# Optimization experiments

Hardware: AMD Instinct MI355X
Metric: run time of the kernel (lower is better)

## Reference

```python
import jax, jax.numpy as jnp
import numpy as np

B, N, C, H = 2, 2048, 768, 12  # batch, seq, dim_self, num_heads
HD = C // H                    # head_dim = 64


def setup_inputs() -> dict:
    key = jax.random.key(0)
    ks = jax.random.split(key, 6)
    s = 0.02
    return {
        "x": jax.random.normal(ks[0], (B, N, C), jnp.float32),
        "mask": jax.random.bernoulli(ks[1], 0.9, (B, N)),  # True = attend (code applies ~mask)
        "Wq": jax.random.normal(ks[2], (C, C), jnp.float32) * s,
        "bq": jnp.zeros((C,), jnp.float32),
        "Wkv": jax.random.normal(ks[3], (C, 2 * C), jnp.float32) * s,
        "bkv": jnp.zeros((2 * C,), jnp.float32),
        "Wp": jax.random.normal(ks[4], (C, C), jnp.float32) * s,
        "bp": jnp.zeros((C,), jnp.float32),
    }


def reference(x, mask, Wq, bq, Wkv, bkv, Wp, bp):
    b, n, c = x.shape
    scale = HD ** -0.5
    # projections (self-attention: y = x)
    q = (x @ Wq + bq).reshape(b, n, H, HD)                  # [b,n,h,d]
    kv = (x @ Wkv + bkv).reshape(b, n, 2, H, HD)            # [b,m,2,h,d]
    k, v = kv[:, :, 0], kv[:, :, 1]                         # [b,m,h,d]
    att = jnp.einsum('bnhd,bmhd->bnmh', q, k) * scale       # [b,n,m,h]
    # mask: [b,m] -> [b,1,m,1]; masked positions get -inf before softmax
    att = jnp.where(mask[:, None, :, None], att, -jnp.inf)
    att = jax.nn.softmax(att, axis=2)                       # softmax over keys (dim m)
    out = jnp.einsum('bnmh,bmhd->bnhd', att, v).reshape(b, n, c)
    out = out @ Wp + bp
    return out, att
```

## Files before the change

kernel.cpp:

```cpp
#include <hip/hip_runtime.h>
#include <hip/hip_bf16.h>

typedef __bf16 bf8 __attribute__((ext_vector_type(8)));
typedef float f4 __attribute__((ext_vector_type(4)));

__device__ __forceinline__ unsigned short f2b(float f) {
  union { __hip_bfloat16 h; unsigned short u; } cv;
  cv.h = __float2bfloat16(f);
  return cv.u;
}

__device__ __forceinline__ float b2f(unsigned short u) {
  union { unsigned int u; float f; } cv;
  cv.u = ((unsigned int)u) << 16;
  return cv.f;
}

__device__ __forceinline__ f4 mfma16(bf8 a, bf8 b, f4 c) {
  return __builtin_amdgcn_mfma_f32_16x16x32_bf16(a, b, c, 0, 0, 0);
}

__device__ __forceinline__ void stage16(const unsigned short* g, unsigned short* lbase, int lane) {
#if __has_builtin(__builtin_amdgcn_global_load_lds)
  __builtin_amdgcn_global_load_lds((const __attribute__((address_space(1))) void*)g,
                                   (__attribute__((address_space(3))) void*)lbase, 16, 0, 0);
#else
  *(bf8*)((char*)lbase + lane * 16) = *(const bf8*)g;
#endif
}

__global__ void k_prept(const float* __restrict__ x, unsigned short* __restrict__ xb,
                        const void* __restrict__ mraw, const float* __restrict__ bq,
                        const float* __restrict__ bkv, float* __restrict__ maskbias,
                        float* __restrict__ biasc,
                        const float* __restrict__ Wq, const float* __restrict__ Wkv,
                        const float* __restrict__ Wp, unsigned short* __restrict__ Wct,
                        unsigned short* __restrict__ Wpt) {
  __shared__ float tile[32][33];
  const int bid = blockIdx.x;
  if (bid < 3072) {
    size_t t = (size_t)bid * 256 + threadIdx.x;
    float4 v = *(const float4*)(x + t * 4);
    ushort4 o;
    o.x = f2b(v.x); o.y = f2b(v.y); o.z = f2b(v.z); o.w = f2b(v.w);
    *(ushort4*)(xb + t * 4) = o;
    return;
  }
  if (bid < 3097) {
    int t = (bid - 3072) * 256 + threadIdx.x;
    const unsigned char* pb = (const unsigned char*)mraw;
    const unsigned int* pd = (const unsigned int*)mraw;
    int isfloat = 0, isbyte = 0;
    for (int i = 0; i < 128; ++i) {
      unsigned int d = pd[i];
      if (d == 0x3f800000u) isfloat = 1;
      if ((d & 0xffffff00u) != 0u && d != 0x3f800000u) isbyte = 1;
    }
    if (t < 4096) {
      int v;
      if (isbyte)       v = pb[t];
      else if (isfloat) v = (((const float*)mraw)[t] != 0.0f);
      else              v = ((const int*)mraw)[t];
      maskbias[t] = v ? 0.0f : -1e30f;
    } else if (t < 4096 + 2304) {
      int j = t - 4096;
      biasc[j] = (j < 768) ? bq[j] : bkv[j - 768];
    }
    return;
  }
  int id = bid - 3097;
  int bx = id % 96, by = id / 96;
  const float* in; unsigned short* out; int Cc, bxl;
  if (bx < 24)      { in = Wq;  out = Wct;                         Cc = 768;  bxl = bx; }
  else if (bx < 72) { in = Wkv; out = Wct + (size_t)768 * 768;     Cc = 1536; bxl = bx - 24; }
  else              { in = Wp;  out = Wpt;                         Cc = 768;  bxl = bx - 72; }
  const int R = 768;
  int c0 = bxl * 32, r0 = by * 32;
  int tx = threadIdx.x & 31, ty = threadIdx.x >> 5;
  for (int j = 0; j < 32; j += 8)
    tile[ty + j][tx] = in[(size_t)(r0 + ty + j) * Cc + c0 + tx];
  __syncthreads();
  for (int j = 0; j < 32; j += 8)
    out[(size_t)(c0 + ty + j) * R + r0 + tx] = f2b(tile[tx][ty + j]);
}

template<int MODE>
__global__ __launch_bounds__(256) void k_gemm(
    const unsigned short* __restrict__ A,
    const unsigned short* __restrict__ Bt,
    const float* __restrict__ bias,
    float* __restrict__ outf,
    unsigned short* __restrict__ qo,
    unsigned short* __restrict__ ko,
    unsigned short* __restrict__ vo,
    int K)
{
  __shared__ unsigned short sm[128 * 136];
  unsigned short* As = sm;
  unsigned short* Bs = sm + 4096;
  const int tid = threadIdx.x;
  const int w = tid >> 6, l = tid & 63;
  const int wr = w >> 1, wc = w & 1;
  const int m0 = blockIdx.y * 128, n0 = blockIdx.x * 128;
  const int lrow = l >> 2, lcol = l & 3;
  const int fr = l & 15, fk = (l >> 4) * 8;
  f4 acc[4][4] = {};

  for (int k0 = 0; k0 < K; k0 += 32) {
    for (int j = 0; j < 2; ++j) {
      int ra = w * 32 + j * 16;
      stage16(A  + (size_t)(m0 + ra + lrow) * K + k0 + lcol * 8, &As[ra * 32], l);
      stage16(Bt + (size_t)(n0 + ra + lrow) * K + k0 + lcol * 8, &Bs[ra * 32], l);
    }
    asm volatile("s_waitcnt vmcnt(0)" ::: "memory");
    __syncthreads();
    bf8 af[4], bfv[4];
#pragma unroll
    for (int i = 0; i < 4; ++i) af[i]  = *(const bf8*)&As[(wr * 64 + i * 16 + fr) * 32 + fk];
#pragma unroll
    for (int i = 0; i < 4; ++i) bfv[i] = *(const bf8*)&Bs[(wc * 64 + i * 16 + fr) * 32 + fk];
#pragma unroll
    for (int i = 0; i < 4; ++i)
#pragma unroll
      for (int j2 = 0; j2 < 4; ++j2)
        acc[i][j2] = mfma16(af[i], bfv[j2], acc[i][j2]);
    __syncthreads();
  }

  const int fg = l >> 4;
  if (MODE == 1) {
#pragma unroll
    for (int j2 = 0; j2 < 4; ++j2) {
      int col = n0 + wc * 64 + j2 * 16 + fr;
      float bv = bias[col];
#pragma unroll
      for (int i = 0; i < 4; ++i) {
        int rbase = m0 + wr * 64 + i * 16 + fg * 4;
#pragma unroll
        for (int r = 0; r < 4; ++r)
          __builtin_nontemporal_store(acc[i][j2][r] + bv, &outf[(size_t)(rbase + r) * 768 + col]);
      }
    }
  } else {
#pragma unroll
    for (int j2 = 0; j2 < 4; ++j2) {
      int colc = wc * 64 + j2 * 16 + fr;
      float bv = bias[n0 + colc];
#pragma unroll
      for (int i = 0; i < 4; ++i)
#pragma unroll
        for (int r = 0; r < 4; ++r)
          sm[(wr * 64 + i * 16 + fg * 4 + r) * 136 + colc] = f2b(acc[i][j2][r] + bv);
    }
    __syncthreads();
#pragma unroll
    for (int it = 0; it < 8; ++it) {
      int flat = it * 2048 + tid * 8;
      int rl = flat >> 7, mc = flat & 127;
      int row = m0 + rl, col = n0 + mc;
      bf8 v = *(const bf8*)&sm[rl * 136 + mc];
      int b = row >> 11, n = row & 2047;
      unsigned short* dst;
      if (col < 768)        { int h = col >> 6;
        dst = qo + (((size_t)b * 12 + h) * 2048 + n) * 64 + (col & 63); }
      else if (col < 1536)  { int c2 = col - 768;  int h = c2 >> 6;
        dst = ko + (((size_t)b * 12 + h) * 2048 + n) * 64 + (c2 & 63); }
      else                  { int c2 = col - 1536; int h = c2 >> 6;
        dst = vo + (((size_t)b * 12 + h) * 2048 + n) * 64 + (c2 & 63); }
      *(bf8*)dst = v;
    }
  }
}

__global__ __launch_bounds__(256) void k_pexptrv(
    const unsigned short* __restrict__ q,
    const unsigned short* __restrict__ kk,
    const float* __restrict__ maskbias,
    unsigned short* __restrict__ Pws,
    float* __restrict__ Lpart,
    const unsigned short* __restrict__ v,
    unsigned short* __restrict__ vT)
{
  __shared__ unsigned short sm[128 * 136];
  const int bid = blockIdx.x;
  const int tid = threadIdx.x;
  if (bid >= 6144) {
    int id = bid - 6144;
    int bx = id & 1, by = (id >> 1) & 63, bz = id >> 7;
    int tx = tid & 31, ty = tid >> 5;
    const unsigned short* src = v + (size_t)bz * 131072;
    unsigned short* dst = vT + (size_t)bz * 131072;
    for (int j = 0; j < 32; j += 8)
      sm[(ty + j) * 33 + tx] = src[(size_t)(by * 32 + ty + j) * 64 + bx * 32 + tx];
    __syncthreads();
    for (int j = 0; j < 32; j += 8)
      dst[(size_t)(bx * 32 + ty + j) * 2048 + by * 32 + tx] = sm[tx * 33 + ty + j];
    return;
  }
  unsigned short* As = sm;
  unsigned short* Bs = sm + 4096;
  const int w = tid >> 6, l = tid & 63;
  const int wr = w >> 1, wc = w & 1;
  const int mt = bid & 15, nt = (bid >> 4) & 15, bh = bid >> 8;
  const int b = bh / 12;
  const int n0 = nt * 128, m0 = mt * 128;
  const int lrow = l >> 2, lcol = l & 3;
  const int fr = l & 15, fg = l >> 4, fk = fg * 8;
  const unsigned short* qh = q + (size_t)bh * 2048 * 64;
  const unsigned short* kh = kk + (size_t)bh * 2048 * 64;
  f4 acc[4][4] = {};

  for (int k0 = 0; k0 < 64; k0 += 32) {
    for (int j = 0; j < 2; ++j) {
      int ra = w * 32 + j * 16;
      stage16(qh + (size_t)(n0 + ra + lrow) * 64 + k0 + lcol * 8, &As[ra * 32], l);
      stage16(kh + (size_t)(m0 + ra + lrow) * 64 + k0 + lcol * 8, &Bs[ra * 32], l);
    }
    asm volatile("s_waitcnt vmcnt(0)" ::: "memory");
    __syncthreads();
    bf8 af[4], bfv[4];
#pragma unroll
    for (int i = 0; i < 4; ++i) af[i]  = *(const bf8*)&As[(wr * 64 + i * 16 + fr) * 32 + fk];
#pragma unroll
    for (int i = 0; i < 4; ++i) bfv[i] = *(const bf8*)&Bs[(wc * 64 + i * 16 + fr) * 32 + fk];
#pragma unroll
    for (int i = 0; i < 4; ++i)
#pragma unroll
      for (int j2 = 0; j2 < 4; ++j2)
        acc[i][j2] = mfma16(af[i], bfv[j2], acc[i][j2]);
    __syncthreads();
  }

  const float scale = 0.125f;
  const float* mbp = maskbias + b * 2048 + m0;
#pragma unroll
  for (int i = 0; i < 4; ++i) {
#pragma unroll
    for (int r = 0; r < 4; ++r) {
      int nl = wr * 64 + i * 16 + fg * 4 + r;
      float rs = 0.0f;
#pragma unroll
      for (int j2 = 0; j2 < 4; ++j2) {
        int ml = wc * 64 + j2 * 16 + fr;
        float p = __expf(fmaf(acc[i][j2][r], scale, mbp[ml]));
        rs += p;
        sm[nl * 136 + ml] = f2b(p);
      }
      rs += __shfl_xor(rs, 1);
      rs += __shfl_xor(rs, 2);
      rs += __shfl_xor(rs, 4);
      rs += __shfl_xor(rs, 8);
      if (fr == 0)
        Lpart[((size_t)bh * 32 + mt * 2 + wc) * 2048 + n0 + nl] = rs;
    }
  }
  __syncthreads();
#pragma unroll
  for (int it = 0; it < 8; ++it) {
    int flat = it * 2048 + tid * 8;
    int row = flat >> 7, mc = flat & 127;
    bf8 vv = *(const bf8*)&sm[row * 136 + mc];
    *(bf8*)(Pws + ((size_t)bh * 2048 + n0 + row) * 2048 + m0 + mc) = vv;
  }
}

__global__ void k_lred(const float* __restrict__ Lpart, float* __restrict__ iLst) {
  int t = blockIdx.x * 256 + threadIdx.x;
  int bh = t >> 11, n = t & 2047;
  float s = 0.0f;
#pragma unroll
  for (int sl = 0; sl < 32; ++sl)
    s += Lpart[((size_t)bh * 32 + sl) * 2048 + n];
  iLst[t] = 1.0f / fmaxf(s, 1e-30f);
}

__global__ __launch_bounds__(256) void k_attwpv(
    const unsigned short* __restrict__ Pws,
    const float* __restrict__ iLst,
    float* __restrict__ att,
    const unsigned short* __restrict__ vT,
    unsigned short* __restrict__ ao)
{
  __shared__ unsigned short smem[6656];
  const int bid = blockIdx.x;
  const int tid = threadIdx.x;
  const int w = tid >> 6, l = tid & 63;

  if (bid < 768) {
    unsigned short* B0 = smem;
    unsigned short* B1 = smem + 2048;
    const int bh = bid % 24, nt = bid / 24;
    const int b = bh / 12, h = bh % 12;
    const int n0 = nt * 64;
    const int lr = l >> 2, lc = (l & 3) * 8;
    const int fr = l & 15, fg = l >> 4, fk = fg * 8;
    const unsigned short* Ph = Pws + (size_t)bh * 2048 * 2048
                             + (size_t)(n0 + w * 16 + fr) * 2048 + fk;
    const unsigned short* vh = vT + (size_t)bh * 64 * 2048;
    f4 acc[4] = {};

    for (int k0 = 0; k0 < 2048; k0 += 64) {
      stage16(vh + (size_t)(w * 16 + lr) * 2048 + k0 + lc,      &B0[(w * 16) * 32], l);
      stage16(vh + (size_t)(w * 16 + lr) * 2048 + k0 + 32 + lc, &B1[(w * 16) * 32], l);
      bf8 a0 = *(const bf8*)(Ph + k0);
      bf8 a1 = *(const bf8*)(Ph + k0 + 32);
      asm volatile("s_waitcnt vmcnt(0)" ::: "memory");
      __syncthreads();
#pragma unroll
      for (int j2 = 0; j2 < 4; ++j2) {
        bf8 bv = *(const bf8*)&B0[(j2 * 16 + fr) * 32 + fk];
        acc[j2] = mfma16(a0, bv, acc[j2]);
      }
#pragma unroll
      for (int j2 = 0; j2 < 4; ++j2) {
        bf8 bv = *(const bf8*)&B1[(j2 * 16 + fr) * 32 + fk];
        acc[j2] = mfma16(a1, bv, acc[j2]);
      }
      __syncthreads();
    }

    float il[4];
#pragma unroll
    for (int r = 0; r < 4; ++r)
      il[r] = iLst[(size_t)bh * 2048 + n0 + w * 16 + fg * 4 + r];
#pragma unroll
    for (int j2 = 0; j2 < 4; ++j2)
#pragma unroll
      for (int r = 0; r < 4; ++r)
        ao[((size_t)(b * 2048) + n0 + w * 16 + fg * 4 + r) * 768 + h * 64 + j2 * 16 + fr]
            = f2b(acc[j2][r] * il[r]);
    return;
  }

  const int idx = (bid - 768) * 4 + w;
  const int b = idx >> 12;
  const int n = (idx >> 1) & 2047;
  const int half = idx & 1;
  const int hq = l >> 4, mg = l & 15;
  unsigned short* sl = smem + w * 1664;

  float iLv[3];
#pragma unroll
  for (int g = 0; g < 3; ++g)
    iLv[g] = iLst[((size_t)(b * 12 + g * 4 + hq)) * 2048 + n];

  for (int c = 0; c < 8; ++c) {
    const int m0 = half * 1024 + c * 128;
#pragma unroll
    for (int g = 0; g < 3; ++g) {
      int h = g * 4 + hq;
      bf8 pv = *(const bf8*)(Pws + ((size_t)(b * 12 + h) * 2048 + n) * 2048 + m0 + mg * 8);
      const unsigned short* pu = (const unsigned short*)&pv;
#pragma unroll
      for (int j = 0; j < 8; ++j)
        sl[mg * 104 + j * 12 + h] = f2b(b2f(pu[j]) * iLv[g]);
    }
    float* dst = att + (((size_t)(b * 2048 + n)) * 2048 + m0) * 12;
#pragma unroll
    for (int it = 0; it < 6; ++it) {
      int f = it * 256 + l * 4;
      int sa = (f / 96) * 104 + f % 96;
      ushort4 s4 = *(const ushort4*)&sl[sa];
      f4 v = {b2f(s4.x), b2f(s4.y), b2f(s4.z), b2f(s4.w)};
      __builtin_nontemporal_store(v, (f4*)(dst + f));
    }
  }
}

extern "C" void kernel_launch(void* const* d_in, const int* in_sizes, int n_in,
                              void* d_out, int out_size, void* d_ws, size_t ws_size,
                              hipStream_t stream) {
  const float* x   = (const float*)d_in[0];
  const void*  msk = d_in[1];
  const float* Wq  = (const float*)d_in[2];
  const float* bq  = (const float*)d_in[3];
  const float* Wkv = (const float*)d_in[4];
  const float* bkv = (const float*)d_in[5];
  const float* Wp  = (const float*)d_in[6];
  const float* bp  = (const float*)d_in[7];
  float* out = (float*)d_out;
  float* att = out + (size_t)2 * 2048 * 768;

  char* ws = (char*)d_ws;
  float* maskbias = (float*)ws;
  float* biasc    = maskbias + 4096;
  unsigned short* xb  = (unsigned short*)(ws + 32768);
  unsigned short* Wct = xb  + (size_t)4096 * 768;
  unsigned short* Wpt = Wct + (size_t)2304 * 768;
  unsigned short* qb  = Wpt + (size_t)768 * 768;
  unsigned short* kb  = qb  + (size_t)3145728;
  unsigned short* vb  = kb  + (size_t)3145728;
  unsigned short* vTb = vb  + (size_t)3145728;
  float* iLstat = (float*)(vTb + (size_t)3145728);
  float* Lpart  = iLstat + 49152;
  unsigned short* Pws = (unsigned short*)(Lpart + (size_t)24 * 32 * 2048);
  unsigned short* ao = xb;

  k_prept<<<dim3(5401), dim3(256), 0, stream>>>(x, xb, msk, bq, bkv, maskbias, biasc,
                                                Wq, Wkv, Wp, Wct, Wpt);
  k_gemm<0><<<dim3(18, 32), dim3(256), 0, stream>>>(xb, Wct, biasc, nullptr, qb, kb, vb, 768);
  k_pexptrv<<<dim3(9216), dim3(256), 0, stream>>>(qb, kb, maskbias, Pws, Lpart, vb, vTb);
  k_lred<<<dim3(192), dim3(256), 0, stream>>>(Lpart, iLstat);
  k_attwpv<<<dim3(2816), dim3(256), 0, stream>>>(Pws, iLstat, att, vTb, ao);
  k_gemm<1><<<dim3(6, 32), dim3(256), 0, stream>>>(ao, Wpt, bp, out, nullptr, nullptr, nullptr, 768);
}
```

Measured before the change: 246.2 us.

## Double-buffer PV staging and prefetch P rows in att-write path

The PV GEMM blocks now use two LDS buffers, so the V tiles and P fragments for the next k-step are loaded while MFMAs run on the current step. This drops one barrier per iteration. The att-expansion blocks issue the loads for the next 128-column chunk of P before converting and storing the current one. Both changes try to hide global load latency, at the cost of more LDS (16 KB) and more registers, which may reduce occupancy.

New measurement: 247.2 us. No clear change (+0.4%).

```diff
diff --git a/kernel.cpp b/kernel.cpp
--- a/kernel.cpp
+++ b/kernel.cpp
@@ -281,14 +281,12 @@
     const unsigned short* __restrict__ vT,
     unsigned short* __restrict__ ao)
 {
-  __shared__ unsigned short smem[6656];
+  __shared__ unsigned short smem[8192];
   const int bid = blockIdx.x;
   const int tid = threadIdx.x;
   const int w = tid >> 6, l = tid & 63;
 
   if (bid < 768) {
-    unsigned short* B0 = smem;
-    unsigned short* B1 = smem + 2048;
     const int bh = bid % 24, nt = bid / 24;
     const int b = bh / 12, h = bh % 12;
     const int n0 = nt * 64;
@@ -299,24 +297,37 @@
     const unsigned short* vh = vT + (size_t)bh * 64 * 2048;
     f4 acc[4] = {};
 
+    stage16(vh + (size_t)(w * 16 + lr) * 2048 + 0 + lc,  smem + (w * 16) * 32, l);
+    stage16(vh + (size_t)(w * 16 + lr) * 2048 + 32 + lc, smem + 2048 + (w * 16) * 32, l);
+    bf8 a0 = *(const bf8*)(Ph + 0);
+    bf8 a1 = *(const bf8*)(Ph + 32);
+    asm volatile("s_waitcnt vmcnt(0)" ::: "memory");
+    __syncthreads();
+
+    int cur = 0;
     for (int k0 = 0; k0 < 2048; k0 += 64) {
-      stage16(vh + (size_t)(w * 16 + lr) * 2048 + k0 + lc,      &B0[(w * 16) * 32], l);
-      stage16(vh + (size_t)(w * 16 + lr) * 2048 + k0 + 32 + lc, &B1[(w * 16) * 32], l);
-      bf8 a0 = *(const bf8*)(Ph + k0);
-      bf8 a1 = *(const bf8*)(Ph + k0 + 32);
+      unsigned short* Bc = smem + cur * 4096;
+      unsigned short* Bn = smem + (cur ^ 1) * 4096;
+      bf8 na0 = a0, na1 = a1;
+      if (k0 + 64 < 2048) {
+        stage16(vh + (size_t)(w * 16 + lr) * 2048 + k0 + 64 + lc, Bn + (w * 16) * 32, l);
+        stage16(vh + (size_t)(w * 16 + lr) * 2048 + k0 + 96 + lc, Bn + 2048 + (w * 16) * 32, l);
+        na0 = *(const bf8*)(Ph + k0 + 64);
+        na1 = *(const bf8*)(Ph + k0 + 96);
+      }
+#pragma unroll
+      for (int j2 = 0; j2 < 4; ++j2) {
+        bf8 bv = *(const bf8*)&Bc[(j2 * 16 + fr) * 32 + fk];
+        acc[j2] = mfma16(a0, bv, acc[j2]);
+      }
+#pragma unroll
+      for (int j2 = 0; j2 < 4; ++j2) {
+        bf8 bv = *(const bf8*)&Bc[2048 + (j2 * 16 + fr) * 32 + fk];
+        acc[j2] = mfma16(a1, bv, acc[j2]);
+      }
       asm volatile("s_waitcnt vmcnt(0)" ::: "memory");
       __syncthreads();
-#pragma unroll
-      for (int j2 = 0; j2 < 4; ++j2) {
-        bf8 bv = *(const bf8*)&B0[(j2 * 16 + fr) * 32 + fk];
-        acc[j2] = mfma16(a0, bv, acc[j2]);
-      }
-#pragma unroll
-      for (int j2 = 0; j2 < 4; ++j2) {
-        bf8 bv = *(const bf8*)&B1[(j2 * 16 + fr) * 32 + fk];
-        acc[j2] = mfma16(a1, bv, acc[j2]);
-      }
-      __syncthreads();
+      a0 = na0; a1 = na1; cur ^= 1;
     }
 
     float il[4];
@@ -338,22 +349,46 @@
   const int half = idx & 1;
   const int hq = l >> 4, mg = l & 15;
   unsigned short* sl = smem + w * 1664;
+  const unsigned short* Pbase = Pws + ((size_t)(b * 12) * 2048 + n) * 2048;
 
   float iLv[3];
 #pragma unroll
   for (int g = 0; g < 3; ++g)
     iLv[g] = iLst[((size_t)(b * 12 + g * 4 + hq)) * 2048 + n];
 
+  bf8 cur0, cur1, cur2;
+  cur0 = *(const bf8*)(Pbase + (size_t)(0 * 4 + hq) * 2048 * 2048 + half * 1024 + mg * 8);
+  cur1 = *(const bf8*)(Pbase + (size_t)(1 * 4 + hq) * 2048 * 2048 + half * 1024 + mg * 8);
+  cur2 = *(const bf8*)(Pbase + (size_t)(2 * 4 + hq) * 2048 * 2048 + half * 1024 + mg * 8);
+
   for (int c = 0; c < 8; ++c) {
     const int m0 = half * 1024 + c * 128;
-#pragma unroll
-    for (int g = 0; g < 3; ++g) {
-      int h = g * 4 + hq;
-      bf8 pv = *(const bf8*)(Pws + ((size_t)(b * 12 + h) * 2048 + n) * 2048 + m0 + mg * 8);
-      const unsigned short* pu = (const unsigned short*)&pv;
+    bf8 nx0 = cur0, nx1 = cur1, nx2 = cur2;
+    if (c < 7) {
+      nx0 = *(const bf8*)(Pbase + (size_t)(0 * 4 + hq) * 2048 * 2048 + m0 + 128 + mg * 8);
+      nx1 = *(const bf8*)(Pbase + (size_t)(1 * 4 + hq) * 2048 * 2048 + m0 + 128 + mg * 8);
+      nx2 = *(const bf8*)(Pbase + (size_t)(2 * 4 + hq) * 2048 * 2048 + m0 + 128 + mg * 8);
+    }
+    {
+      const unsigned short* pu = (const unsigned short*)&cur0;
+      int h = 0 * 4 + hq;
 #pragma unroll
       for (int j = 0; j < 8; ++j)
-        sl[mg * 104 + j * 12 + h] = f2b(b2f(pu[j]) * iLv[g]);
+        sl[mg * 104 + j * 12 + h] = f2b(b2f(pu[j]) * iLv[0]);
+    }
+    {
+      const unsigned short* pu = (const unsigned short*)&cur1;
+      int h = 1 * 4 + hq;
+#pragma unroll
+      for (int j = 0; j < 8; ++j)
+        sl[mg * 104 + j * 12 + h] = f2b(b2f(pu[j]) * iLv[1]);
+    }
+    {
+      const unsigned short* pu = (const unsigned short*)&cur2;
+      int h = 2 * 4 + hq;
+#pragma unroll
+      for (int j = 0; j < 8; ++j)
+        sl[mg * 104 + j * 12 + h] = f2b(b2f(pu[j]) * iLv[2]);
     }
     float* dst = att + (((size_t)(b * 2048 + n)) * 2048 + m0) * 12;
 #pragma unroll
@@ -364,6 +399,7 @@
       f4 v = {b2f(s4.x), b2f(s4.y), b2f(s4.z), b2f(s4.w)};
       __builtin_nontemporal_store(v, (f4*)(dst + f));
     }
+    cur0 = nx0; cur1 = nx1; cur2 = nx2;
   }
 }
 
```
